# Performance work log

Measured on AMD Instinct MI355X. Metric: run time of the kernel, lower is better.

Reference implementation:

```python
import jax, jax.numpy as jnp
import numpy as np

N_HEADS = 16
ROPE_BASE = 10000.0


def apply_rope(x):
    # x: (b, h, t, d); rotate interleaved pairs along last dim, positions = t axis
    b, h, t, d = x.shape
    theta = 1.0 / (ROPE_BASE ** (jnp.arange(0, d, 2, dtype=jnp.float32) / d))  # (d/2,)
    ang = jnp.arange(t, dtype=jnp.float32)[:, None] * theta[None, :]           # (t, d/2)
    cos = jnp.cos(ang)[None, None]  # (1,1,t,d/2)
    sin = jnp.sin(ang)[None, None]
    xp = x.reshape(b, h, t, d // 2, 2)
    x0, x1 = xp[..., 0], xp[..., 1]
    o0 = x0 * cos - x1 * sin
    o1 = x1 * cos + x0 * sin
    return jnp.stack([o0, o1], axis=-1).reshape(b, h, t, d)


def setup_inputs() -> dict:
    key = jax.random.key(0)
    k1, k2, k3 = jax.random.split(key, 3)
    B, T, C = 2, 2048, 1024
    x = jax.random.normal(k1, (B, T, C), dtype=jnp.float32)
    w_qkv = jax.random.normal(k2, (3 * C, C), dtype=jnp.float32) * (1.0 / np.sqrt(C))
    w_proj = jax.random.normal(k3, (C, C), dtype=jnp.float32) * (1.0 / np.sqrt(C))
    return {"x": x, "w_qkv": w_qkv, "w_proj": w_proj}


def reference(x, w_qkv, w_proj):
    B, T, C = x.shape
    H = N_HEADS
    D = C // H
    # fused QKV projection: (b,t,3C)
    qkv = x @ w_qkv.T
    qkv = qkv.reshape(B, T, 3, H, D).transpose(2, 0, 3, 1, 4)  # (3, b, h, t, d)
    q, k, v = qkv[0], qkv[1], qkv[2]
    q = apply_rope(q)
    k = apply_rope(k)
    scale = 1.0 / jnp.sqrt(jnp.float32(D))
    scores = jnp.einsum('bhqd,bhkd->bhqk', q, k) * scale  # (b,h,t,t)
    causal = jnp.tril(jnp.ones((T, T), dtype=bool))
    scores = jnp.where(causal[None, None], scores, jnp.finfo(scores.dtype).min)
    attn = jax.nn.softmax(scores, axis=-1)
    y = jnp.einsum('bhqk,bhkd->bhqd', attn, v)  # (b,h,t,d)
    y = y.transpose(0, 2, 1, 3).reshape(B, T, C)
    return y @ w_proj.T
```

## Files before the change

### kernel.cpp

```cpp
#include <hip/hip_runtime.h>
#include <math.h>

#define B_ 2
#define T_ 2048
#define C_ 1024
#define H_ 16
#define D_ 64
#define NX_ 4194304
#define NWQ_ 3145728
#define NWP_ 1048576

typedef unsigned short u16;
typedef unsigned int u32;
typedef __bf16 bf16x8 __attribute__((ext_vector_type(8)));
typedef _Float16 f16x8 __attribute__((ext_vector_type(8)));
typedef __fp16 fp16x2 __attribute__((ext_vector_type(2)));
typedef float f32x4 __attribute__((ext_vector_type(4)));
typedef u16 u16x4 __attribute__((ext_vector_type(4)));

__device__ __forceinline__ u16 f2bf(float f) {
    union { float f; u32 u; } v; v.f = f;
    u32 r = v.u + 0x7fffu + ((v.u >> 16) & 1u);
    return (u16)(r >> 16);
}

#define GLD_LDS(g, l) \
    __builtin_amdgcn_global_load_lds( \
        (const __attribute__((address_space(1))) u32*)(const void*)(g), \
        (__attribute__((address_space(3))) u32*)(void*)(l), 16, 0, 0)

__global__ __launch_bounds__(256) void cast_all(const float* __restrict__ x,
                                                const float* __restrict__ wq,
                                                const float* __restrict__ wp,
                                                u16* __restrict__ out) {
    const int i = (blockIdx.x * 256 + threadIdx.x) * 4;
    const float* src;
    int off;
    if (i < NX_) { src = x; off = i; }
    else if (i < NX_ + NWQ_) { src = wq; off = i - NX_; }
    else { src = wp; off = i - NX_ - NWQ_; }
    float4 v = *(const float4*)(src + off);
    u16x4 o;
    o.x = f2bf(v.x); o.y = f2bf(v.y); o.z = f2bf(v.z); o.w = f2bf(v.w);
    *(u16x4*)(out + i) = o;
}

template <int EPI>
__global__ __launch_bounds__(256) void gemm64(const u16* __restrict__ A,
                                              const u16* __restrict__ Bm,
                                              float* __restrict__ OutF,
                                              u16* __restrict__ qb,
                                              u16* __restrict__ kb,
                                              u16* __restrict__ vt,
                                              int M, int N, int K) {
    __shared__ u16 As[128 * 64];
    __shared__ u16 Bs[128 * 64];
    const int tid = threadIdx.x;
    const int lane = tid & 63;
    const int wave = tid >> 6;
    const int wm = (wave >> 1) * 64;
    const int wn = (wave & 1) * 64;
    const int m0 = blockIdx.y * 128;
    const int n0 = blockIdx.x * 128;

    const int rl = lane >> 3;
    const int sg = ((lane & 7) ^ rl) * 8;
    const u16* gA[4]; const u16* gB[4];
    u16 *lA[4], *lB[4];
    #pragma unroll
    for (int c = 0; c < 4; ++c) {
        const int ca = wave * 4 + c;
        gA[c] = A + (size_t)(m0 + ca * 8 + rl) * K + sg;
        gB[c] = Bm + (size_t)(n0 + ca * 8 + rl) * K + sg;
        lA[c] = As + ca * 512;
        lB[c] = Bs + ca * 512;
    }

    const int col = lane & 15;
    const int quad = lane >> 4;
    int aoff[2][4], boff[2][4];
    #pragma unroll
    for (int ks = 0; ks < 2; ++ks)
        #pragma unroll
        for (int i = 0; i < 4; ++i) {
            const int m = wm + i * 16 + col;
            aoff[ks][i] = (m >> 3) * 512 + (m & 7) * 64 +
                          ((((ks << 2) | quad)) ^ (m & 7)) * 8;
            const int n = wn + i * 16 + col;
            boff[ks][i] = (n >> 3) * 512 + (n & 7) * 64 +
                          ((((ks << 2) | quad)) ^ (n & 7)) * 8;
        }

    f32x4 acc[4][4] = {};
    for (int k0 = 0; k0 < K; k0 += 64) {
        __syncthreads();
        #pragma unroll
        for (int c = 0; c < 4; ++c) {
            GLD_LDS(gA[c] + k0, lA[c]);
            GLD_LDS(gB[c] + k0, lB[c]);
        }
        __syncthreads();
        #pragma unroll
        for (int ks = 0; ks < 2; ++ks) {
            bf16x8 a[4], b[4];
            #pragma unroll
            for (int i = 0; i < 4; ++i) a[i] = *(const bf16x8*)(As + aoff[ks][i]);
            #pragma unroll
            for (int j = 0; j < 4; ++j) b[j] = *(const bf16x8*)(Bs + boff[ks][j]);
            #pragma unroll
            for (int i = 0; i < 4; ++i)
                #pragma unroll
                for (int j = 0; j < 4; ++j)
                    acc[i][j] = __builtin_amdgcn_mfma_f32_16x16x32_bf16(
                        a[i], b[j], acc[i][j], 0, 0, 0);
        }
    }

    const int rq = quad * 4;
    if (EPI == 0) {
        #pragma unroll
        for (int i = 0; i < 4; ++i)
            #pragma unroll
            for (int j = 0; j < 4; ++j)
                #pragma unroll
                for (int r = 0; r < 4; ++r)
                    OutF[(size_t)(m0 + wm + i * 16 + rq + r) * N +
                         n0 + wn + j * 16 + col] = acc[i][j][r];
    } else {
        const int sslot = m0 >> 10;
        #pragma unroll
        for (int i = 0; i < 4; ++i) {
            const int gm = m0 + wm + i * 16 + rq;
            const int hh = (gm >> 6) & 15;
            const int dbase = gm & 63;
            #pragma unroll
            for (int j = 0; j < 4; ++j) {
                const int gt = n0 + wn + j * 16 + col;
                const int bb = gt >> 11;
                const int t = gt & (T_ - 1);
                const int bh = bb * H_ + hh;
                if (sslot < 2) {
                    const float tf = (float)t;
                    u16x4 ov;
                    #pragma unroll
                    for (int p = 0; p < 2; ++p) {
                        const float ip = (float)((dbase >> 1) + p);
                        const float theta = __expf(-0.2878231366f * ip);
                        const float ang = tf * theta;
                        float sn, cs; __sincosf(ang, &sn, &cs);
                        const float x0 = acc[i][j][2 * p];
                        const float x1 = acc[i][j][2 * p + 1];
                        ov[2 * p]     = f2bf(x0 * cs - x1 * sn);
                        ov[2 * p + 1] = f2bf(x1 * cs + x0 * sn);
                    }
                    u16* dst = (sslot == 0 ? qb : kb) +
                               ((size_t)bh * T_ + t) * D_ + dbase;
                    *(u16x4*)dst = ov;
                } else {
                    #pragma unroll
                    for (int r = 0; r < 4; ++r) {
                        union { _Float16 h; u16 u; } cv;
                        cv.h = (_Float16)acc[i][j][r];
                        vt[((size_t)bh * D_ + dbase + r) * T_ + t] = cv.u;
                    }
                }
            }
        }
    }
}

__global__ __launch_bounds__(256) void attn_mfma(const u16* __restrict__ qb,
                                                 const u16* __restrict__ kb,
                                                 const u16* __restrict__ vtg,
                                                 u16* __restrict__ y) {
    __shared__ u16 Ks[2][8 * 512];
    __shared__ u16 Vt[2][8 * 512];
    __shared__ u16 Ps[4][32 * 72];
    const int id = blockIdx.x;
    const int qt = (id < 256) ? (15 - (id >> 5)) : ((id - 256) >> 5);
    const int bh = id & 31;
    const int b = bh >> 4, h = bh & 15;
    const int q0 = qt * 128;
    const int tid = threadIdx.x;
    const int lane = tid & 63;
    const int wave = tid >> 6;
    const int col = lane & 15;
    const int quad = lane >> 4;

    const u16* qbase = qb + ((size_t)bh * T_ + q0 + wave * 32) * D_;
    bf16x8 qf[2][2];
    #pragma unroll
    for (int qh = 0; qh < 2; ++qh)
        #pragma unroll
        for (int ks = 0; ks < 2; ++ks)
            qf[qh][ks] = *(const bf16x8*)(qbase + (qh * 16 + col) * D_ +
                                          ks * 32 + quad * 8);

    f32x4 o[2][4] = {};
    float lsum[2] = {0.0f, 0.0f};

    const int rl = lane >> 3;
    const int sg = ((lane & 7) ^ rl) * 8;
    const u16* kg[2]; const u16* vg[2];
    int lco[2];
    #pragma unroll
    for (int e = 0; e < 2; ++e) {
        const int ca = 2 * wave + e;
        kg[e] = kb + ((size_t)bh * T_ + ca * 8 + rl) * D_ + sg;
        vg[e] = vtg + ((size_t)bh * D_ + ca * 8 + rl) * T_ + sg;
        lco[e] = ca * 512;
    }
    u16* Pw = &Ps[wave][0];

    int koff[2][4];
    #pragma unroll
    for (int ks = 0; ks < 2; ++ks)
        #pragma unroll
        for (int n = 0; n < 4; ++n) {
            const int rr = n * 16 + col;
            koff[ks][n] = (rr >> 3) * 512 + (rr & 7) * 64 +
                          ((((ks << 2) | quad)) ^ (rr & 7)) * 8;
        }

    const int nchunks = 2 * qt + 2;
    #pragma unroll
    for (int e = 0; e < 2; ++e) {
        GLD_LDS(kg[e], &Ks[0][lco[e]]);
        GLD_LDS(vg[e], &Vt[0][lco[e]]);
    }

    for (int ci = 0; ci < nchunks; ++ci) {
        const int buf = ci & 1;
        const int j0 = ci * 64;
        __syncthreads();
        if (ci + 1 < nchunks) {
            const size_t j1 = (size_t)(ci + 1) * 64;
            #pragma unroll
            for (int e = 0; e < 2; ++e) {
                GLD_LDS(kg[e] + j1 * D_, &Ks[buf ^ 1][lco[e]]);
                GLD_LDS(vg[e] + j1, &Vt[buf ^ 1][lco[e]]);
            }
        }

        f32x4 s[2][4] = {};
        #pragma unroll
        for (int ks = 0; ks < 2; ++ks) {
            #pragma unroll
            for (int n = 0; n < 4; ++n) {
                const bf16x8 kf = *(const bf16x8*)(&Ks[buf][koff[ks][n]]);
                #pragma unroll
                for (int qh = 0; qh < 2; ++qh)
                    s[qh][n] = __builtin_amdgcn_mfma_f32_16x16x32_bf16(
                        kf, qf[qh][ks], s[qh][n], 0, 0, 0);
            }
        }

        const bool diag = (ci >= nchunks - 2);
        #pragma unroll
        for (int qh = 0; qh < 2; ++qh) {
            const int qrow = q0 + wave * 32 + qh * 16 + col;
            #pragma unroll
            for (int n = 0; n < 4; ++n) {
                float p[4];
                #pragma unroll
                for (int r = 0; r < 4; ++r) {
                    const float xv = s[qh][n][r] * 0.1803368801f;
                    float pv = __builtin_amdgcn_exp2f(fminf(xv, 80.0f));
                    if (diag && (j0 + n * 16 + quad * 4 + r > qrow)) pv = 0.0f;
                    p[r] = pv;
                    lsum[qh] += pv;
                }
                union { fp16x2 h[2]; u32 u[2]; } pk;
                pk.h[0] = __builtin_amdgcn_cvt_pkrtz(p[0], p[1]);
                pk.h[1] = __builtin_amdgcn_cvt_pkrtz(p[2], p[3]);
                *(uint2*)(Pw + (qh * 16 + col) * 72 + n * 16 + quad * 4) =
                    make_uint2(pk.u[0], pk.u[1]);
            }
        }

        #pragma unroll
        for (int ks = 0; ks < 2; ++ks) {
            f16x8 pf[2];
            #pragma unroll
            for (int qh = 0; qh < 2; ++qh)
                pf[qh] = *(const f16x8*)(Pw + (qh * 16 + col) * 72 +
                                         ks * 32 + quad * 8);
            #pragma unroll
            for (int n = 0; n < 4; ++n) {
                const f16x8 vf = *(const f16x8*)(&Vt[buf][koff[ks][n]]);
                #pragma unroll
                for (int qh = 0; qh < 2; ++qh)
                    o[qh][n] = __builtin_amdgcn_mfma_f32_16x16x32_f16(
                        pf[qh], vf, o[qh][n], 0, 0, 0);
            }
        }
    }

    #pragma unroll
    for (int qh = 0; qh < 2; ++qh) {
        float l = lsum[qh];
        l += __shfl_xor(l, 16);
        l += __shfl_xor(l, 32);
        const float inv = 1.0f / l;
        float invr[4];
        #pragma unroll
        for (int r = 0; r < 4; ++r)
            invr[r] = __shfl(inv, quad * 4 + r);
        #pragma unroll
        for (int r = 0; r < 4; ++r) {
            const int row = q0 + wave * 32 + qh * 16 + quad * 4 + r;
            u16* yp = y + (size_t)(b * T_ + row) * C_ + h * D_;
            #pragma unroll
            for (int n = 0; n < 4; ++n)
                yp[n * 16 + col] = f2bf(o[qh][n][r] * invr[r]);
        }
    }
}

extern "C" void kernel_launch(void* const* d_in, const int* in_sizes, int n_in,
                              void* d_out, int out_size, void* d_ws, size_t ws_size,
                              hipStream_t stream) {
    const float* x      = (const float*)d_in[0];
    const float* w_qkv  = (const float*)d_in[1];
    const float* w_proj = (const float*)d_in[2];
    float* out = (float*)d_out;

    const int M = B_ * T_;
    u16* xb  = (u16*)d_ws;
    u16* wqb = xb + NX_;
    u16* wpb = wqb + NWQ_;
    u16* qb  = wpb + NWP_;
    u16* kb  = qb + NX_;
    u16* vt  = kb + NX_;
    u16* yb  = vt + NX_;

    cast_all<<<(NX_ + NWQ_ + NWP_) / 1024, 256, 0, stream>>>(x, w_qkv, w_proj, xb);

    gemm64<1><<<dim3(M / 128, 3 * C_ / 128), 256, 0, stream>>>(
        wqb, xb, nullptr, qb, kb, vt, 3 * C_, M, C_);

    attn_mfma<<<512, 256, 0, stream>>>(qb, kb, vt, yb);

    gemm64<0><<<dim3(C_ / 128, M / 128), 256, 0, stream>>>(
        yb, wpb, out, nullptr, nullptr, nullptr, M, C_, C_);
}
```

Before: 190.0 us.

## Precompute RoPE table, halve attention query tile, pass P through shuffles

```diff
diff --git a/kernel.cpp b/kernel.cpp
--- a/kernel.cpp
+++ b/kernel.cpp
@@ -32,8 +32,23 @@
 __global__ __launch_bounds__(256) void cast_all(const float* __restrict__ x,
                                                 const float* __restrict__ wq,
                                                 const float* __restrict__ wp,
-                                                u16* __restrict__ out) {
-    const int i = (blockIdx.x * 256 + threadIdx.x) * 4;
+                                                u16* __restrict__ out,
+                                                float* __restrict__ tab) {
+    const int bid = blockIdx.x;
+    if (bid >= 8192) {
+        const int k = (bid - 8192) * 256 + threadIdx.x;
+        #pragma unroll
+        for (int e = 0; e < 2; ++e) {
+            const int pidx = 2 * k + e;
+            const int t = pidx >> 5, i = pidx & 31;
+            const float theta = __expf(-0.2878231366f * (float)i);
+            float sn, cs;
+            __sincosf((float)t * theta, &sn, &cs);
+            *(float2*)(tab + pidx * 2) = make_float2(cs, sn);
+        }
+        return;
+    }
+    const int i = (bid * 256 + threadIdx.x) * 4;
     const float* src;
     int off;
     if (i < NX_) { src = x; off = i; }
@@ -52,6 +67,7 @@
                                               u16* __restrict__ qb,
                                               u16* __restrict__ kb,
                                               u16* __restrict__ vt,
+                                              const float* __restrict__ tab,
                                               int M, int N, int K) {
     __shared__ u16 As[128 * 64];
     __shared__ u16 Bs[128 * 64];
@@ -140,19 +156,12 @@
                 const int t = gt & (T_ - 1);
                 const int bh = bb * H_ + hh;
                 if (sslot < 2) {
-                    const float tf = (float)t;
+                    const float4 cs4 = *(const float4*)(tab + t * 64 + dbase);
                     u16x4 ov;
-                    #pragma unroll
-                    for (int p = 0; p < 2; ++p) {
-                        const float ip = (float)((dbase >> 1) + p);
-                        const float theta = __expf(-0.2878231366f * ip);
-                        const float ang = tf * theta;
-                        float sn, cs; __sincosf(ang, &sn, &cs);
-                        const float x0 = acc[i][j][2 * p];
-                        const float x1 = acc[i][j][2 * p + 1];
-                        ov[2 * p]     = f2bf(x0 * cs - x1 * sn);
-                        ov[2 * p + 1] = f2bf(x1 * cs + x0 * sn);
-                    }
+                    ov[0] = f2bf(acc[i][j][0] * cs4.x - acc[i][j][1] * cs4.y);
+                    ov[1] = f2bf(acc[i][j][1] * cs4.x + acc[i][j][0] * cs4.y);
+                    ov[2] = f2bf(acc[i][j][2] * cs4.z - acc[i][j][3] * cs4.w);
+                    ov[3] = f2bf(acc[i][j][3] * cs4.z + acc[i][j][2] * cs4.w);
                     u16* dst = (sslot == 0 ? qb : kb) +
                                ((size_t)bh * T_ + t) * D_ + dbase;
                     *(u16x4*)dst = ov;
@@ -175,29 +184,25 @@
                                                  u16* __restrict__ y) {
     __shared__ u16 Ks[2][8 * 512];
     __shared__ u16 Vt[2][8 * 512];
-    __shared__ u16 Ps[4][32 * 72];
     const int id = blockIdx.x;
-    const int qt = (id < 256) ? (15 - (id >> 5)) : ((id - 256) >> 5);
+    const int qt = (id < 512) ? (31 - (id >> 5)) : ((id - 512) >> 5);
     const int bh = id & 31;
     const int b = bh >> 4, h = bh & 15;
-    const int q0 = qt * 128;
+    const int q0 = qt * 64;
     const int tid = threadIdx.x;
     const int lane = tid & 63;
     const int wave = tid >> 6;
     const int col = lane & 15;
     const int quad = lane >> 4;
 
-    const u16* qbase = qb + ((size_t)bh * T_ + q0 + wave * 32) * D_;
-    bf16x8 qf[2][2];
-    #pragma unroll
-    for (int qh = 0; qh < 2; ++qh)
-        #pragma unroll
-        for (int ks = 0; ks < 2; ++ks)
-            qf[qh][ks] = *(const bf16x8*)(qbase + (qh * 16 + col) * D_ +
-                                          ks * 32 + quad * 8);
-
-    f32x4 o[2][4] = {};
-    float lsum[2] = {0.0f, 0.0f};
+    const u16* qbase = qb + ((size_t)bh * T_ + q0 + wave * 16) * D_;
+    bf16x8 qf[2];
+    #pragma unroll
+    for (int ks = 0; ks < 2; ++ks)
+        qf[ks] = *(const bf16x8*)(qbase + col * D_ + ks * 32 + quad * 8);
+
+    f32x4 o[4] = {};
+    float lsum = 0.0f;
 
     const int rl = lane >> 3;
     const int sg = ((lane & 7) ^ rl) * 8;
@@ -210,7 +215,6 @@
         vg[e] = vtg + ((size_t)bh * D_ + ca * 8 + rl) * T_ + sg;
         lco[e] = ca * 512;
     }
-    u16* Pw = &Ps[wave][0];
 
     int koff[2][4];
     #pragma unroll
@@ -222,7 +226,12 @@
                           ((((ks << 2) | quad)) ^ (rr & 7)) * 8;
         }
 
-    const int nchunks = 2 * qt + 2;
+    const int srcA = col + ((quad & 1) << 5);
+    const int srcB = srcA + 16;
+    const bool hi = (quad >> 1) != 0;
+    const int qrow = q0 + wave * 16 + col;
+
+    const int nchunks = qt + 1;
     #pragma unroll
     for (int e = 0; e < 2; ++e) {
         GLD_LDS(kg[e], &Ks[0][lco[e]]);
@@ -242,78 +251,71 @@
             }
         }
 
-        f32x4 s[2][4] = {};
-        #pragma unroll
-        for (int ks = 0; ks < 2; ++ks) {
+        f32x4 s[4] = {};
+        #pragma unroll
+        for (int ks = 0; ks < 2; ++ks)
             #pragma unroll
             for (int n = 0; n < 4; ++n) {
                 const bf16x8 kf = *(const bf16x8*)(&Ks[buf][koff[ks][n]]);
-                #pragma unroll
-                for (int qh = 0; qh < 2; ++qh)
-                    s[qh][n] = __builtin_amdgcn_mfma_f32_16x16x32_bf16(
-                        kf, qf[qh][ks], s[qh][n], 0, 0, 0);
-            }
-        }
-
-        const bool diag = (ci >= nchunks - 2);
-        #pragma unroll
-        for (int qh = 0; qh < 2; ++qh) {
-            const int qrow = q0 + wave * 32 + qh * 16 + col;
-            #pragma unroll
-            for (int n = 0; n < 4; ++n) {
-                float p[4];
-                #pragma unroll
-                for (int r = 0; r < 4; ++r) {
-                    const float xv = s[qh][n][r] * 0.1803368801f;
-                    float pv = __builtin_amdgcn_exp2f(fminf(xv, 80.0f));
-                    if (diag && (j0 + n * 16 + quad * 4 + r > qrow)) pv = 0.0f;
-                    p[r] = pv;
-                    lsum[qh] += pv;
-                }
-                union { fp16x2 h[2]; u32 u[2]; } pk;
-                pk.h[0] = __builtin_amdgcn_cvt_pkrtz(p[0], p[1]);
-                pk.h[1] = __builtin_amdgcn_cvt_pkrtz(p[2], p[3]);
-                *(uint2*)(Pw + (qh * 16 + col) * 72 + n * 16 + quad * 4) =
-                    make_uint2(pk.u[0], pk.u[1]);
-            }
+                s[n] = __builtin_amdgcn_mfma_f32_16x16x32_bf16(
+                    kf, qf[ks], s[n], 0, 0, 0);
+            }
+
+        const bool diag = (ci == nchunks - 1);
+        u32 pk[4][2];
+        #pragma unroll
+        for (int n = 0; n < 4; ++n) {
+            float p[4];
+            #pragma unroll
+            for (int r = 0; r < 4; ++r) {
+                float pv = __builtin_amdgcn_exp2f(s[n][r] * 0.1803368801f);
+                if (diag && (j0 + n * 16 + quad * 4 + r > qrow)) pv = 0.0f;
+                p[r] = pv;
+                lsum += pv;
+            }
+            union { fp16x2 h; u32 u; } k0, k1;
+            k0.h = __builtin_amdgcn_cvt_pkrtz(p[0], p[1]);
+            k1.h = __builtin_amdgcn_cvt_pkrtz(p[2], p[3]);
+            pk[n][0] = k0.u;
+            pk[n][1] = k1.u;
         }
 
         #pragma unroll
         for (int ks = 0; ks < 2; ++ks) {
-            f16x8 pf[2];
-            #pragma unroll
-            for (int qh = 0; qh < 2; ++qh)
-                pf[qh] = *(const f16x8*)(Pw + (qh * 16 + col) * 72 +
-                                         ks * 32 + quad * 8);
+            const int nl = 2 * ks, nh = nl + 1;
+            const u32 w0a = __shfl(pk[nl][0], srcA), w0b = __shfl(pk[nh][0], srcA);
+            const u32 w1a = __shfl(pk[nl][1], srcA), w1b = __shfl(pk[nh][1], srcA);
+            const u32 w2a = __shfl(pk[nl][0], srcB), w2b = __shfl(pk[nh][0], srcB);
+            const u32 w3a = __shfl(pk[nl][1], srcB), w3b = __shfl(pk[nh][1], srcB);
+            union { u32 u[4]; f16x8 v; } af;
+            af.u[0] = hi ? w0b : w0a;
+            af.u[1] = hi ? w1b : w1a;
+            af.u[2] = hi ? w2b : w2a;
+            af.u[3] = hi ? w3b : w3a;
             #pragma unroll
             for (int n = 0; n < 4; ++n) {
                 const f16x8 vf = *(const f16x8*)(&Vt[buf][koff[ks][n]]);
-                #pragma unroll
-                for (int qh = 0; qh < 2; ++qh)
-                    o[qh][n] = __builtin_amdgcn_mfma_f32_16x16x32_f16(
-                        pf[qh], vf, o[qh][n], 0, 0, 0);
-            }
-        }
-    }
-
-    #pragma unroll
-    for (int qh = 0; qh < 2; ++qh) {
-        float l = lsum[qh];
-        l += __shfl_xor(l, 16);
-        l += __shfl_xor(l, 32);
-        const float inv = 1.0f / l;
-        float invr[4];
-        #pragma unroll
-        for (int r = 0; r < 4; ++r)
-            invr[r] = __shfl(inv, quad * 4 + r);
-        #pragma unroll
-        for (int r = 0; r < 4; ++r) {
-            const int row = q0 + wave * 32 + qh * 16 + quad * 4 + r;
-            u16* yp = y + (size_t)(b * T_ + row) * C_ + h * D_;
-            #pragma unroll
-            for (int n = 0; n < 4; ++n)
-                yp[n * 16 + col] = f2bf(o[qh][n][r] * invr[r]);
-        }
+                o[n] = __builtin_amdgcn_mfma_f32_16x16x32_f16(
+                    af.v, vf, o[n], 0, 0, 0);
+            }
+        }
+    }
+
+    float l = lsum;
+    l += __shfl_xor(l, 16);
+    l += __shfl_xor(l, 32);
+    const float inv = 1.0f / l;
+    float invr[4];
+    #pragma unroll
+    for (int r = 0; r < 4; ++r)
+        invr[r] = __shfl(inv, quad * 4 + r);
+    #pragma unroll
+    for (int r = 0; r < 4; ++r) {
+        const int row = q0 + wave * 16 + quad * 4 + r;
+        u16* yp = y + (size_t)(b * T_ + row) * C_ + h * D_;
+        #pragma unroll
+        for (int n = 0; n < 4; ++n)
+            yp[n * 16 + col] = f2bf(o[n][r] * invr[r]);
     }
 }
 
@@ -333,14 +335,15 @@
     u16* kb  = qb + NX_;
     u16* vt  = kb + NX_;
     u16* yb  = vt + NX_;
-
-    cast_all<<<(NX_ + NWQ_ + NWP_) / 1024, 256, 0, stream>>>(x, w_qkv, w_proj, xb);
+    float* tab = (float*)(yb + NX_);
+
+    cast_all<<<8192 + 128, 256, 0, stream>>>(x, w_qkv, w_proj, xb, tab);
 
     gemm64<1><<<dim3(M / 128, 3 * C_ / 128), 256, 0, stream>>>(
-        wqb, xb, nullptr, qb, kb, vt, 3 * C_, M, C_);
-
-    attn_mfma<<<512, 256, 0, stream>>>(qb, kb, vt, yb);
+        wqb, xb, nullptr, qb, kb, vt, tab, 3 * C_, M, C_);
+
+    attn_mfma<<<1024, 256, 0, stream>>>(qb, kb, vt, yb);
 
     gemm64<0><<<dim3(C_ / 128, M / 128), 256, 0, stream>>>(
-        yb, wpb, out, nullptr, nullptr, nullptr, M, C_, C_);
-}
+        yb, wpb, out, nullptr, nullptr, nullptr, nullptr, M, C_, C_);
+}
```

Result: faster. 179.4 us (-5.6%).
